# Kernel tuning notes

Measured on AMD Instinct MI355X. Metric: run time of the kernel, lower is better.

Reference implementation:

```python
import jax, jax.numpy as jnp
import numpy as np

B, S, D, H = 2, 2048, 1024, 16
DK = D // H  # 64


def setup_inputs() -> dict:
    key = jax.random.key(0)
    ks = jax.random.split(key, 4)
    scale = 1.0 / np.sqrt(D)
    return {
        "q_input": jax.random.normal(ks[0], (B, S, D), dtype=jnp.float32),
        "W_q": jax.random.normal(ks[1], (D, D), dtype=jnp.float32) * scale,
        "b_q": jnp.zeros((D,), dtype=jnp.float32),
        "W_k": jax.random.normal(ks[2], (D, D), dtype=jnp.float32) * scale,
        "b_k": jnp.zeros((D,), dtype=jnp.float32),
        "W_v": jax.random.normal(ks[3], (D, D), dtype=jnp.float32) * scale,
        "b_v": jnp.zeros((D,), dtype=jnp.float32),
    }


def reference(q_input, W_q, b_q, W_k, b_k, W_v, b_v):
    # Self-attention: k_input and v_input default to q_input in the torch module.
    # nn.Linear computes x @ W.T + b
    q = q_input @ W_q.T + b_q
    k = q_input @ W_k.T + b_k
    v = q_input @ W_v.T + b_v

    # [B,S,D] -> [B,H,S,DK]
    def split_heads(x):
        return x.reshape(B, S, H, DK).transpose(0, 2, 1, 3)

    qh, kh, vh = split_heads(q), split_heads(k), split_heads(v)

    # scores [B,H,S,S]; causal mask added BEFORE scaling (as in source; -inf invariant)
    scores = jnp.einsum("bhqd,bhkd->bhqk", qh, kh)
    causal = jnp.tril(jnp.ones((S, S), dtype=bool))
    scores = jnp.where(causal[None, None], scores, -jnp.inf)
    scores = scores / jnp.sqrt(jnp.float32(DK))
    probs = jax.nn.softmax(scores, axis=-1)
    z = jnp.einsum("bhqk,bhkd->bhqd", probs, vh)  # [B,H,S,DK]
    # [B,H,S,DK] -> [B,S,H,DK] -> [B,S,D]
    return z.transpose(0, 2, 1, 3).reshape(B, S, D)
```

## Files before the change

kernel.cpp:

```cpp
#include <hip/hip_runtime.h>
#include <hip/hip_bf16.h>
#include <stdint.h>

typedef __attribute__((ext_vector_type(8))) short short8;
typedef __attribute__((ext_vector_type(4))) short short4v;
typedef __attribute__((ext_vector_type(4))) float f32x4;
typedef __attribute__((ext_vector_type(16))) float f32x16;

#define B_ 2
#define S_ 2048
#define D_ 1024
#define H_ 16
#define DK_ 64
#define M_ (B_*S_)

#define WS_QKV   0
#define WS_XB    12582912
#define WS_WB    16777216

#define QSCALE (0.125f * 1.44269504088896f)

#define GLL16(g, l) __builtin_amdgcn_global_load_lds( \
    (const __attribute__((address_space(1))) void*)(g), \
    (__attribute__((address_space(3))) void*)(l), 16, 0, 0)

#define WAIT_VM0 asm volatile("s_waitcnt vmcnt(0)" ::: "memory")
#define WAIT_VM4 asm volatile("s_waitcnt vmcnt(4)" ::: "memory")
#define WAIT_VM8 asm volatile("s_waitcnt vmcnt(8)" ::: "memory")
#define WAIT_LGKM0 asm volatile("s_waitcnt lgkmcnt(0)" ::: "memory")
#define BARRIER_RAW asm volatile("s_barrier" ::: "memory")

static __device__ __forceinline__ short f2bf(float f){
  union { float f; unsigned u; } x; x.f = f;
  unsigned r = x.u + 0x7fff + ((x.u >> 16) & 1);
  return (short)(r >> 16);
}

__global__ __launch_bounds__(256) void cvt_bf16(
    const float* __restrict__ X,  const float* __restrict__ Wq,
    const float* __restrict__ Wk, const float* __restrict__ Wv,
    short* __restrict__ ws)
{
  const int z = blockIdx.z;
  const float* src; short* dst; int n;
  if (z == 0)      { src = X;  dst = ws + WS_XB;               n = M_*D_; }
  else if (z == 1) { src = Wq; dst = ws + WS_WB;               n = D_*D_; }
  else if (z == 2) { src = Wk; dst = ws + WS_WB + D_*D_;       n = D_*D_; }
  else             { src = Wv; dst = ws + WS_WB + 2*(D_*D_);   n = D_*D_; }
  const int stride = gridDim.x * blockDim.x * 4;
  for (int i = (blockIdx.x * blockDim.x + threadIdx.x) * 4; i < n; i += stride) {
    float4 v = *(const float4*)(src + i);
    short4v o;
    o.x = f2bf(v.x); o.y = f2bf(v.y); o.z = f2bf(v.z); o.w = f2bf(v.w);
    *(short4v*)(dst + i) = o;
  }
}

__global__ __launch_bounds__(512, 2) void qkv_gemm(
    const short* __restrict__ ws_in,
    const float* __restrict__ bq, const float* __restrict__ bk,
    const float* __restrict__ bv, short* __restrict__ qkv)
{
  const int z = blockIdx.z;
  const short* X  = ws_in + WS_XB;
  const short* Wm = ws_in + WS_WB + (size_t)z * (D_*D_);
  short* out = qkv + (size_t)z * (M_*D_);

  __shared__ __align__(16) short lds[65536];

  const int t = threadIdx.x;
  const int w = t >> 6, lane = t & 63;
  const int quad = lane >> 4, l16 = lane & 15;
  const int wm = w >> 2, wn = w & 3;
  const int m0 = blockIdx.y * 256, n0 = blockIdx.x * 256;

  const int rl = t >> 2;
  const int sl = (t & 3) ^ (rl & 3);
  const short* sA0 = X  + (size_t)(m0 + rl) * D_ + sl*8;
  const short* sA1 = sA0 + (size_t)128 * D_;
  const short* sB0 = Wm + (size_t)(n0 + rl) * D_ + sl*8;
  const short* sB1 = sB0 + (size_t)128 * D_;
  const int ldsw = w << 9;

  const int swz = quad ^ (l16 & 3);

  int aoff[8], boff[4];
  #pragma unroll
  for (int mf=0; mf<8; mf++) aoff[mf] = (wm*128 + mf*16 + l16)*32 + swz*8;
  #pragma unroll
  for (int nf=0; nf<4; nf++) boff[nf] = (wn*64 + nf*16 + l16)*32 + swz*8;

  f32x4 acc[8][4];
  #pragma unroll
  for (int i=0;i<8;i++)
    #pragma unroll
    for (int j=0;j<4;j++) acc[i][j] = (f32x4){0.f,0.f,0.f,0.f};

  #pragma unroll
  for (int p=0;p<4;p++){
    GLL16(sA0 + p*32, lds + p*16384 + ldsw);
    GLL16(sA1 + p*32, lds + p*16384 + 4096 + ldsw);
    GLL16(sB0 + p*32, lds + p*16384 + 8192 + ldsw);
    GLL16(sB1 + p*32, lds + p*16384 + 12288 + ldsw);
  }
  WAIT_VM8;
  BARRIER_RAW;

  short8 F0[12], F1[12];
  #pragma unroll
  for (int nf=0; nf<4; nf++) F0[8+nf] = *(const short8*)(lds + 8192 + boff[nf]);
  #pragma unroll
  for (int mf=0; mf<8; mf++) F0[mf]   = *(const short8*)(lds + aoff[mf]);
  WAIT_LGKM0;
  BARRIER_RAW;

#define QKV_WINDOW(KT, CUR, NXT)                                           \
  {                                                                        \
    const int kt_ = (KT);                                                  \
    if (kt_ + 1 < 32){                                                     \
      const short* nb = lds + ((kt_+1)&3)*16384;                           \
      _Pragma("unroll")                                                    \
      for (int nf=0; nf<4; nf++)                                           \
        NXT[8+nf] = *(const short8*)(nb + 8192 + boff[nf]);                \
      _Pragma("unroll")                                                    \
      for (int mf=0; mf<8; mf++)                                           \
        NXT[mf] = *(const short8*)(nb + aoff[mf]);                         \
    }                                                                      \
    if (kt_ + 4 < 32){                                                     \
      const int ko = (kt_+4)*32;                                           \
      short* tb = lds + (kt_&3)*16384;                                     \
      GLL16(sA0 + ko, tb + ldsw);                                          \
      GLL16(sA1 + ko, tb + 4096 + ldsw);                                   \
      GLL16(sB0 + ko, tb + 8192 + ldsw);                                   \
      GLL16(sB1 + ko, tb + 12288 + ldsw);                                  \
    }                                                                      \
    __builtin_amdgcn_s_setprio(1);                                         \
    _Pragma("unroll")                                                      \
    for (int mf=0; mf<8; mf++)                                             \
      _Pragma("unroll")                                                    \
      for (int nf=0; nf<4; nf++)                                           \
        acc[mf][nf] = __builtin_amdgcn_mfma_f32_16x16x32_bf16(             \
            CUR[mf], CUR[8+nf], acc[mf][nf], 0,0,0);                       \
    __builtin_amdgcn_s_setprio(0);                                         \
    WAIT_LGKM0;                                                            \
    if      (kt_ <= 27) { WAIT_VM8; }                                      \
    else if (kt_ == 28) { WAIT_VM4; }                                      \
    else if (kt_ == 29) { WAIT_VM0; }                                      \
    if (kt_ < 31) BARRIER_RAW;                                             \
  }

  for (int kt = 0; kt < 32; kt += 2){
    QKV_WINDOW(kt,     F0, F1);
    QKV_WINDOW(kt + 1, F1, F0);
  }
#undef QKV_WINDOW

  __syncthreads();

  if (z != 2) {
    const float scale = (z==0) ? QSCALE : 1.0f;
    const float* bias = (z==0) ? bq : bk;
    float bv4[4];
    #pragma unroll
    for (int nf=0; nf<4; nf++) bv4[nf] = bias[n0 + wn*64 + nf*16 + l16];
    short* ep = lds;
    #pragma unroll
    for (int p=0; p<2; p++){
      if (wm == p){
        #pragma unroll
        for (int mf=0; mf<8; mf++)
          #pragma unroll
          for (int nf=0; nf<4; nf++)
            #pragma unroll
            for (int i=0; i<4; i++)
              ep[(mf*16 + quad*4 + i)*264 + wn*64 + nf*16 + l16] =
                  f2bf((acc[mf][nf][i] + bv4[nf]) * scale);
      }
      __syncthreads();
      #pragma unroll
      for (int it=0; it<8; it++){
        const int cid = it*512 + t;
        const int row = cid >> 5, cc = cid & 31;
        short8 vv = *(const short8*)(ep + row*264 + cc*8);
        const int m = m0 + p*128 + row, bidx = m >> 11, s = m & 2047;
        const int n = n0 + cc*8, h = n >> 6, dd = n & 63;
        *(short8*)(out + (((size_t)(bidx*H_ + h))*S_ + s)*DK_ + dd) = vv;
      }
      __syncthreads();
    }
  } else {
    float bv4[4];
    #pragma unroll
    for (int nf=0; nf<4; nf++) bv4[nf] = bv[n0 + wn*64 + nf*16 + l16];
    short* ep = lds;
    #pragma unroll
    for (int p=0; p<2; p++){
      if (wm == p){
        #pragma unroll
        for (int mf=0; mf<8; mf++)
          #pragma unroll
          for (int nf=0; nf<4; nf++)
            #pragma unroll
            for (int i=0; i<4; i++)
              ep[(wn*64 + nf*16 + l16)*136 + mf*16 + quad*4 + i] =
                  f2bf(acc[mf][nf][i] + bv4[nf]);
      }
      __syncthreads();
      #pragma unroll
      for (int it=0; it<8; it++){
        const int cid = it*512 + t;
        const int row = cid >> 4, cc = cid & 15;
        short8 vv = *(const short8*)(ep + row*136 + cc*8);
        const int n = n0 + row, h = n >> 6, dd = n & 63;
        const int m0p = m0 + p*128;
        const int bidx = m0p >> 11;
        const int s = (m0p & 2047) + cc*8;
        *(short8*)(out + (((size_t)(bidx*H_ + h))*DK_ + dd)*S_ + s) = vv;
      }
      __syncthreads();
    }
  }
}

static __device__ __forceinline__ void attn_steps(
    const int nSteps, const int I0, const int nA, const int q0w,
    const short8* __restrict__ bqv,
    const short* __restrict__ K, const short* __restrict__ VT,
    short (*Kbuf)[4096], short (*Vbuf)[4096],
    const int g, const int w, const int l32, const int h, const int xrow,
    const int row0, const int sc8,
    f32x16& o0, f32x16& o1, float& lsum)
{
  for (int j = 0; j < nSteps; ++j){
    const int I  = I0 + j;
    const int gt = 2*I + g;
    const int kb = (2*j + g)*64;
    const bool active = (kb <= q0w + 31);
    const short* Kc = &Kbuf[gt & 3][0];
    const short* Vc = &Vbuf[gt & 3][0];

    short8 ak[8], vk[8];
    if (active){
      #pragma unroll
      for (int dc=0; dc<4; dc++){
        const int xk = ((dc*2 + h) ^ xrow)*8;
        ak[dc]   = *(const short8*)(Kc + l32*64 + xk);
        ak[4+dc] = *(const short8*)(Kc + (32 + l32)*64 + xk);
        vk[dc]   = *(const short8*)(Vc + l32*64 + xk);
        vk[4+dc] = *(const short8*)(Vc + (32 + l32)*64 + xk);
      }
    }
    WAIT_LGKM0;
    BARRIER_RAW;

    #pragma unroll
    for (int q=0; q<2; q++){
      const int gp = 2*I + 4 + q;
      if (gp < 34){
        const int kbp = (gp < nA ? gp : gp - nA) * 64;
        GLL16(K  + (size_t)(kbp + row0)*DK_ + sc8, &Kbuf[gp & 3][0] + w*512);
        GLL16(VT + (size_t)row0*S_ + kbp + sc8,    &Vbuf[gp & 3][0] + w*512);
      }
    }

    if (active){
      f32x16 s[2];
      #pragma unroll
      for (int e=0;e<16;e++){ s[0][e] = 0.f; s[1][e] = 0.f; }
      #pragma unroll
      for (int dc=0; dc<4; dc++){
        s[0] = __builtin_amdgcn_mfma_f32_32x32x16_bf16(ak[dc],   bqv[dc], s[0], 0,0,0);
        s[1] = __builtin_amdgcn_mfma_f32_32x32x16_bf16(ak[4+dc], bqv[dc], s[1], 0,0,0);
      }

      if (kb + 63 > q0w) {
        const int qg = q0w + l32;
        #pragma unroll
        for (int r=0; r<16; r++){
          const int k0 = kb + (r&3) + 8*(r>>2) + 4*h;
          if (k0      > qg) s[0][r] = -3.0e38f;
          if (k0 + 32 > qg) s[1][r] = -3.0e38f;
        }
      }

      short8 pf[4];
      #pragma unroll
      for (int mk=0; mk<2; mk++){
        #pragma unroll
        for (int u=0; u<2; u++){
          float p0 = __builtin_amdgcn_exp2f(s[mk][8*u+0]);
          float p1 = __builtin_amdgcn_exp2f(s[mk][8*u+1]);
          float p2 = __builtin_amdgcn_exp2f(s[mk][8*u+2]);
          float p3 = __builtin_amdgcn_exp2f(s[mk][8*u+3]);
          float p4 = __builtin_amdgcn_exp2f(s[mk][8*u+4]);
          float p5 = __builtin_amdgcn_exp2f(s[mk][8*u+5]);
          float p6 = __builtin_amdgcn_exp2f(s[mk][8*u+6]);
          float p7 = __builtin_amdgcn_exp2f(s[mk][8*u+7]);
          lsum += ((p0+p1)+(p2+p3)) + ((p4+p5)+(p6+p7));
          unsigned X0, X1, Y0, Y1;
          asm("v_cvt_pk_bf16_f32 %0, %1, %2" : "=v"(X0) : "v"(p0), "v"(p1));
          asm("v_cvt_pk_bf16_f32 %0, %1, %2" : "=v"(X1) : "v"(p2), "v"(p3));
          asm("v_cvt_pk_bf16_f32 %0, %1, %2" : "=v"(Y0) : "v"(p4), "v"(p5));
          asm("v_cvt_pk_bf16_f32 %0, %1, %2" : "=v"(Y1) : "v"(p6), "v"(p7));
          asm("v_permlane32_swap_b32 %0, %1" : "+v"(X0), "+v"(Y0));
          asm("v_permlane32_swap_b32 %0, %1" : "+v"(X1), "+v"(Y1));
          union { unsigned u4[4]; short8 s8; } pp;
          pp.u4[0] = X0; pp.u4[1] = X1; pp.u4[2] = Y0; pp.u4[3] = Y1;
          pf[mk*2 + u] = pp.s8;
        }
      }

      #pragma unroll
      for (int kk=0; kk<4; kk++){
        o0 = __builtin_amdgcn_mfma_f32_32x32x16_bf16(pf[kk], vk[kk],   o0, 0,0,0);
        o1 = __builtin_amdgcn_mfma_f32_32x32x16_bf16(pf[kk], vk[4+kk], o1, 0,0,0);
      }
    }

    if      (I < 15)  { WAIT_VM4; }
    else if (I == 15) { WAIT_VM0; }
    if (I < 16) BARRIER_RAW;
  }
}

static __device__ __forceinline__ void attn_merge_store(
    float* __restrict__ out, const int bb, const int hh, const int qbase,
    const int w, const int wq, const int lane, const int l32, const int h,
    f32x16& o0, f32x16& o1, float& lsum,
    float (*ms)[64][33])
{
  if (w >= 4){
    #pragma unroll
    for (int e=0; e<16; e++){
      ms[wq][lane][e]    = o0[e];
      ms[wq][lane][16+e] = o1[e];
    }
    ms[wq][lane][32] = lsum;
  }
  WAIT_LGKM0;
  BARRIER_RAW;
  if (w < 4){
    #pragma unroll
    for (int e=0; e<16; e++){
      o0[e] += ms[wq][lane][e];
      o1[e] += ms[wq][lane][16+e];
    }
    float ls = lsum + ms[wq][lane][32];
    float rs = ls + __shfl_xor(ls, 32, 64);
    float linv = 1.0f / rs;
    #pragma unroll
    for (int r=0; r<16; r++){
      const int qrow = (r&3) + 8*(r>>2) + 4*h;
      const float lw = __shfl(linv, qrow, 64);
      float* dst = out + ((size_t)bb*S_ + (qbase + qrow))*D_ + hh*DK_;
      dst[l32]      = o0[r] * lw;
      dst[32 + l32] = o1[r] * lw;
    }
  }
  #pragma unroll
  for (int e=0; e<16; e++){ o0[e] = 0.f; o1[e] = 0.f; }
  lsum = 0.f;
}

__global__ __launch_bounds__(512, 1) void attn(
    const short* __restrict__ qkv, float* __restrict__ out)
{
  const int id = blockIdx.x;
  const int slot = id >> 3;
  const int bh = (id & 7) + 8*(slot & 3);
  const int p  = slot >> 2;
  const int nA = 2*p + 2;

  const short* Q  = qkv + (size_t)bh * (S_*DK_);
  const short* K  = Q + (size_t)(M_*D_);
  const short* VT = qkv + (size_t)(2*M_*D_) + (size_t)bh * (DK_*S_);

  __shared__ short Kbuf[4][4096];
  __shared__ short Vbuf[4][4096];
  __shared__ float ms[4][64][33];

  const int t = threadIdx.x;
  const int w = t >> 6, lane = t & 63;
  const int g = w >> 2, wq = w & 3;
  const int l32 = lane & 31, h = lane >> 5;
  const int xrow = l32 & 7;

  const int qA0 = p*128 + wq*32;
  const int qB0 = (15-p)*128 + wq*32;

  short8 bqA[4], bqB[4];
  #pragma unroll
  for (int dc=0; dc<4; dc++){
    bqA[dc] = *(const short8*)(Q + (size_t)(qA0 + l32)*DK_ + dc*16 + h*8);
    bqB[dc] = *(const short8*)(Q + (size_t)(qB0 + l32)*DK_ + dc*16 + h*8);
  }
  #pragma unroll
  for (int dc=0; dc<4; dc++){
    asm volatile("" : "+v"(bqA[dc]));
    asm volatile("" : "+v"(bqB[dc]));
  }

  const int r8   = lane >> 3;
  const int sc8  = ((lane & 7) ^ r8) * 8;
  const int row0 = w*8 + r8;

  #pragma unroll
  for (int pt=0; pt<4; pt++){
    const int kb = (pt < nA ? pt : pt - nA) * 64;
    GLL16(K  + (size_t)(kb + row0)*DK_ + sc8, &Kbuf[pt][0] + w*512);
    GLL16(VT + (size_t)row0*S_ + kb + sc8,    &Vbuf[pt][0] + w*512);
  }
  WAIT_VM4;
  BARRIER_RAW;

  f32x16 o0, o1;
  #pragma unroll
  for (int e=0; e<16; e++){ o0[e] = 0.f; o1[e] = 0.f; }
  float lsum = 0.f;
  const int bb = bh >> 4, hh = bh & 15;

  attn_steps(nA/2, 0, nA, qA0, bqA, K, VT, Kbuf, Vbuf,
             g, w, l32, h, xrow, row0, sc8, o0, o1, lsum);
  attn_merge_store(out, bb, hh, qA0, w, wq, lane, l32, h, o0, o1, lsum, ms);

  attn_steps(17 - nA/2, nA/2, nA, qB0, bqB, K, VT, Kbuf, Vbuf,
             g, w, l32, h, xrow, row0, sc8, o0, o1, lsum);
  attn_merge_store(out, bb, hh, qB0, w, wq, lane, l32, h, o0, o1, lsum, ms);
}

extern "C" void kernel_launch(void* const* d_in, const int* in_sizes, int n_in,
                              void* d_out, int out_size, void* d_ws, size_t ws_size,
                              hipStream_t stream)
{
  (void)in_sizes; (void)n_in; (void)out_size; (void)ws_size;
  const float* X  = (const float*)d_in[0];
  const float* Wq = (const float*)d_in[1];
  const float* bq = (const float*)d_in[2];
  const float* Wk = (const float*)d_in[3];
  const float* bk = (const float*)d_in[4];
  const float* Wv = (const float*)d_in[5];
  const float* bv = (const float*)d_in[6];
  short* ws  = (short*)d_ws;
  float* out = (float*)d_out;

  dim3 g0(1024, 1, 4);
  cvt_bf16<<<g0, dim3(256,1,1), 0, stream>>>(X, Wq, Wk, Wv, ws);
  dim3 g1(D_/256, M_/256, 3);
  qkv_gemm<<<g1, dim3(512,1,1), 0, stream>>>(ws, bq, bk, bv, ws + WS_QKV);
  dim3 g2(256, 1);
  attn<<<g2, dim3(512,1,1), 0, stream>>>(ws + WS_QKV, out);
}
```

Measured before the change: 157.8 us.

## Use 4 waves per QKV GEMM block with 128x128 per-wave tiles

The QKV projection GEMM goes from 8 waves of 128x64 sub-tiles to 4 waves of 128x128 sub-tiles for the same 256x256 block tile. Each wave now issues twice as many global-to-LDS loads, with vmcnt waits widened to match, and runs 64 MFMAs per k-step instead of 32. This raises register-level reuse of A/B fragments and cuts per-block LDS read traffic. In exchange it halves the waves available to hide latency and greatly raises register pressure (64 accumulators plus 32 fragment registers), which could cause spills or low occupancy.

```diff
diff --git a/kernel.cpp b/kernel.cpp
--- a/kernel.cpp
+++ b/kernel.cpp
@@ -24,9 +24,10 @@
     (const __attribute__((address_space(1))) void*)(g), \
     (__attribute__((address_space(3))) void*)(l), 16, 0, 0)
 
-#define WAIT_VM0 asm volatile("s_waitcnt vmcnt(0)" ::: "memory")
-#define WAIT_VM4 asm volatile("s_waitcnt vmcnt(4)" ::: "memory")
-#define WAIT_VM8 asm volatile("s_waitcnt vmcnt(8)" ::: "memory")
+#define WAIT_VM0  asm volatile("s_waitcnt vmcnt(0)" ::: "memory")
+#define WAIT_VM4  asm volatile("s_waitcnt vmcnt(4)" ::: "memory")
+#define WAIT_VM8  asm volatile("s_waitcnt vmcnt(8)" ::: "memory")
+#define WAIT_VM16 asm volatile("s_waitcnt vmcnt(16)" ::: "memory")
 #define WAIT_LGKM0 asm volatile("s_waitcnt lgkmcnt(0)" ::: "memory")
 #define BARRIER_RAW asm volatile("s_barrier" ::: "memory")
 
@@ -56,7 +57,7 @@
   }
 }
 
-__global__ __launch_bounds__(512, 2) void qkv_gemm(
+__global__ __launch_bounds__(256, 1) void qkv_gemm(
     const short* __restrict__ ws_in,
     const float* __restrict__ bq, const float* __restrict__ bk,
     const float* __restrict__ bv, short* __restrict__ qkv)
@@ -71,44 +72,42 @@
   const int t = threadIdx.x;
   const int w = t >> 6, lane = t & 63;
   const int quad = lane >> 4, l16 = lane & 15;
-  const int wm = w >> 2, wn = w & 3;
+  const int wm = w >> 1, wn = w & 1;
   const int m0 = blockIdx.y * 256, n0 = blockIdx.x * 256;
 
-  const int rl = t >> 2;
-  const int sl = (t & 3) ^ (rl & 3);
-  const short* sA0 = X  + (size_t)(m0 + rl) * D_ + sl*8;
-  const short* sA1 = sA0 + (size_t)128 * D_;
-  const short* sB0 = Wm + (size_t)(n0 + rl) * D_ + sl*8;
-  const short* sB1 = sB0 + (size_t)128 * D_;
-  const int ldsw = w << 9;
+  const int rA  = lane >> 2;
+  const int slc = ((lane & 3) ^ (rA & 3)) * 8;
+  const short* sA = X  + (size_t)(m0 + w*64 + rA) * D_ + slc;
+  const short* sB = Wm + (size_t)(n0 + w*64 + rA) * D_ + slc;
+  const int dA = w*2048;
 
   const int swz = quad ^ (l16 & 3);
-
-  int aoff[8], boff[4];
+  int aoff[8], boff[8];
   #pragma unroll
   for (int mf=0; mf<8; mf++) aoff[mf] = (wm*128 + mf*16 + l16)*32 + swz*8;
   #pragma unroll
-  for (int nf=0; nf<4; nf++) boff[nf] = (wn*64 + nf*16 + l16)*32 + swz*8;
-
-  f32x4 acc[8][4];
+  for (int nf=0; nf<8; nf++) boff[nf] = 8192 + (wn*128 + nf*16 + l16)*32 + swz*8;
+
+  f32x4 acc[8][8];
   #pragma unroll
   for (int i=0;i<8;i++)
     #pragma unroll
-    for (int j=0;j<4;j++) acc[i][j] = (f32x4){0.f,0.f,0.f,0.f};
+    for (int j=0;j<8;j++) acc[i][j] = (f32x4){0.f,0.f,0.f,0.f};
 
   #pragma unroll
   for (int p=0;p<4;p++){
-    GLL16(sA0 + p*32, lds + p*16384 + ldsw);
-    GLL16(sA1 + p*32, lds + p*16384 + 4096 + ldsw);
-    GLL16(sB0 + p*32, lds + p*16384 + 8192 + ldsw);
-    GLL16(sB1 + p*32, lds + p*16384 + 12288 + ldsw);
-  }
-  WAIT_VM8;
+    #pragma unroll
+    for (int j=0;j<4;j++){
+      GLL16(sA + (size_t)j*16*D_ + p*32, lds + p*16384 + dA + j*512);
+      GLL16(sB + (size_t)j*16*D_ + p*32, lds + p*16384 + 8192 + dA + j*512);
+    }
+  }
+  WAIT_VM16;
   BARRIER_RAW;
 
-  short8 F0[12], F1[12];
-  #pragma unroll
-  for (int nf=0; nf<4; nf++) F0[8+nf] = *(const short8*)(lds + 8192 + boff[nf]);
+  short8 F0[16], F1[16];
+  #pragma unroll
+  for (int nf=0; nf<8; nf++) F0[8+nf] = *(const short8*)(lds + boff[nf]);
   #pragma unroll
   for (int mf=0; mf<8; mf++) F0[mf]   = *(const short8*)(lds + aoff[mf]);
   WAIT_LGKM0;
@@ -120,8 +119,8 @@
     if (kt_ + 1 < 32){                                                     \
       const short* nb = lds + ((kt_+1)&3)*16384;                           \
       _Pragma("unroll")                                                    \
-      for (int nf=0; nf<4; nf++)                                           \
-        NXT[8+nf] = *(const short8*)(nb + 8192 + boff[nf]);                \
+      for (int nf=0; nf<8; nf++)                                           \
+        NXT[8+nf] = *(const short8*)(nb + boff[nf]);                       \
       _Pragma("unroll")                                                    \
       for (int mf=0; mf<8; mf++)                                           \
         NXT[mf] = *(const short8*)(nb + aoff[mf]);                         \
@@ -129,22 +128,23 @@
     if (kt_ + 4 < 32){                                                     \
       const int ko = (kt_+4)*32;                                           \
       short* tb = lds + (kt_&3)*16384;                                     \
-      GLL16(sA0 + ko, tb + ldsw);                                          \
-      GLL16(sA1 + ko, tb + 4096 + ldsw);                                   \
-      GLL16(sB0 + ko, tb + 8192 + ldsw);                                   \
-      GLL16(sB1 + ko, tb + 12288 + ldsw);                                  \
+      _Pragma("unroll")                                                    \
+      for (int j=0;j<4;j++){                                               \
+        GLL16(sA + (size_t)j*16*D_ + ko, tb + dA + j*512);                 \
+        GLL16(sB + (size_t)j*16*D_ + ko, tb + 8192 + dA + j*512);          \
+      }                                                                    \
     }                                                                      \
     __builtin_amdgcn_s_setprio(1);                                         \
     _Pragma("unroll")                                                      \
     for (int mf=0; mf<8; mf++)                                             \
       _Pragma("unroll")                                                    \
-      for (int nf=0; nf<4; nf++)                                           \
+      for (int nf=0; nf<8; nf++)                                           \
         acc[mf][nf] = __builtin_amdgcn_mfma_f32_16x16x32_bf16(             \
             CUR[mf], CUR[8+nf], acc[mf][nf], 0,0,0);                       \
     __builtin_amdgcn_s_setprio(0);                                         \
     WAIT_LGKM0;                                                            \
-    if      (kt_ <= 27) { WAIT_VM8; }                                      \
-    else if (kt_ == 28) { WAIT_VM4; }                                      \
+    if      (kt_ <= 27) { WAIT_VM16; }                                     \
+    else if (kt_ == 28) { WAIT_VM8; }                                      \
     else if (kt_ == 29) { WAIT_VM0; }                                      \
     if (kt_ < 31) BARRIER_RAW;                                             \
   }
@@ -160,9 +160,9 @@
   if (z != 2) {
     const float scale = (z==0) ? QSCALE : 1.0f;
     const float* bias = (z==0) ? bq : bk;
-    float bv4[4];
-    #pragma unroll
-    for (int nf=0; nf<4; nf++) bv4[nf] = bias[n0 + wn*64 + nf*16 + l16];
+    float bv8[8];
+    #pragma unroll
+    for (int nf=0; nf<8; nf++) bv8[nf] = bias[n0 + wn*128 + nf*16 + l16];
     short* ep = lds;
     #pragma unroll
     for (int p=0; p<2; p++){
@@ -170,16 +170,16 @@
         #pragma unroll
         for (int mf=0; mf<8; mf++)
           #pragma unroll
-          for (int nf=0; nf<4; nf++)
+          for (int nf=0; nf<8; nf++)
             #pragma unroll
             for (int i=0; i<4; i++)
-              ep[(mf*16 + quad*4 + i)*264 + wn*64 + nf*16 + l16] =
-                  f2bf((acc[mf][nf][i] + bv4[nf]) * scale);
+              ep[(mf*16 + quad*4 + i)*264 + wn*128 + nf*16 + l16] =
+                  f2bf((acc[mf][nf][i] + bv8[nf]) * scale);
       }
       __syncthreads();
       #pragma unroll
-      for (int it=0; it<8; it++){
-        const int cid = it*512 + t;
+      for (int it=0; it<16; it++){
+        const int cid = it*256 + t;
         const int row = cid >> 5, cc = cid & 31;
         short8 vv = *(const short8*)(ep + row*264 + cc*8);
         const int m = m0 + p*128 + row, bidx = m >> 11, s = m & 2047;
@@ -189,9 +189,9 @@
       __syncthreads();
     }
   } else {
-    float bv4[4];
-    #pragma unroll
-    for (int nf=0; nf<4; nf++) bv4[nf] = bv[n0 + wn*64 + nf*16 + l16];
+    float bv8[8];
+    #pragma unroll
+    for (int nf=0; nf<8; nf++) bv8[nf] = bv[n0 + wn*128 + nf*16 + l16];
     short* ep = lds;
     #pragma unroll
     for (int p=0; p<2; p++){
@@ -199,16 +199,16 @@
         #pragma unroll
         for (int mf=0; mf<8; mf++)
           #pragma unroll
-          for (int nf=0; nf<4; nf++)
+          for (int nf=0; nf<8; nf++)
             #pragma unroll
             for (int i=0; i<4; i++)
-              ep[(wn*64 + nf*16 + l16)*136 + mf*16 + quad*4 + i] =
-                  f2bf(acc[mf][nf][i] + bv4[nf]);
+              ep[(wn*128 + nf*16 + l16)*136 + mf*16 + quad*4 + i] =
+                  f2bf(acc[mf][nf][i] + bv8[nf]);
       }
       __syncthreads();
       #pragma unroll
-      for (int it=0; it<8; it++){
-        const int cid = it*512 + t;
+      for (int it=0; it<16; it++){
+        const int cid = it*256 + t;
         const int row = cid >> 4, cc = cid & 15;
         short8 vv = *(const short8*)(ep + row*136 + cc*8);
         const int n = n0 + row, h = n >> 6, dd = n & 63;
@@ -446,7 +446,7 @@
   dim3 g0(1024, 1, 4);
   cvt_bf16<<<g0, dim3(256,1,1), 0, stream>>>(X, Wq, Wk, Wv, ws);
   dim3 g1(D_/256, M_/256, 3);
-  qkv_gemm<<<g1, dim3(512,1,1), 0, stream>>>(ws, bq, bk, bv, ws + WS_QKV);
+  qkv_gemm<<<g1, dim3(256,1,1), 0, stream>>>(ws, bq, bk, bv, ws + WS_QKV);
   dim3 g2(256, 1);
   attn<<<g2, dim3(512,1,1), 0, stream>>>(ws + WS_QKV, out);
 }
```

After: 278.4 us. 76.5% more time.
